# Optimization experiments

Measured on AMD Instinct MI355X. Metric: run time of the kernel, lower is better.

## Reference

```python
import jax, jax.numpy as jnp
import numpy as np

N = 50000
NEG_SLOPE = 0.2

def _gat_layer(x, src, dst, W, a_src, a_dst, b):
    # x: [N, Fin], W: [Fin, Fout], a_src/a_dst: [Fout], b: [Fout]
    h = x @ W                                  # [N, Fout]
    alpha_src = h @ a_src                      # [N]
    alpha_dst = h @ a_dst                      # [N]
    e = alpha_src[src] + alpha_dst[dst]        # [E]
    e = jnp.where(e > 0, e, NEG_SLOPE * e)     # leaky_relu
    # segment softmax over incoming edges of each dst node
    m = jax.ops.segment_max(e, dst, num_segments=N)
    w = jnp.exp(e - m[dst])
    denom = jax.ops.segment_sum(w, dst, num_segments=N) + jnp.asarray(1e-16, e.dtype)
    alpha = w / denom[dst]                     # [E]
    out = jax.ops.segment_sum(alpha[:, None] * h[src], dst, num_segments=N)
    return out + b

def setup_inputs() -> dict:
    key = jax.random.key(0)
    ks = jax.random.split(key, 10)
    x = jax.random.normal(ks[0], (N, 128), dtype=jnp.float32)
    edge_index = jax.random.randint(ks[1], (2, 800000), 0, N, dtype=jnp.int64)
    def glorot(k, shape):
        fan = shape[0] + (shape[1] if len(shape) > 1 else 1)
        s = jnp.sqrt(6.0 / fan)
        return jax.random.uniform(k, shape, jnp.float32, -s, s)
    return {
        "x": x,
        "edge_index": edge_index,
        "W1": glorot(ks[2], (128, 64)),
        "a1_src": glorot(ks[3], (64,)),
        "a1_dst": glorot(ks[4], (64,)),
        "b1": jnp.zeros((64,), jnp.float32),
        "W2": glorot(ks[5], (64, 64)),
        "a2_src": glorot(ks[6], (64,)),
        "a2_dst": glorot(ks[7], (64,)),
        "b2": jnp.zeros((64,), jnp.float32),
    }

def reference(x, edge_index, W1, a1_src, a1_dst, b1, W2, a2_src, a2_dst, b2):
    loops = jnp.arange(N, dtype=edge_index.dtype)
    src = jnp.concatenate([edge_index[0], loops])  # add self-loops (PyG default)
    dst = jnp.concatenate([edge_index[1], loops])
    h = _gat_layer(x, src, dst, W1, a1_src, a1_dst, b1)
    h = jax.nn.relu(h)
    out = _gat_layer(h, src, dst, W2, a2_src, a2_dst, b2)
    return out
```

## Files before the change

### kernel.cpp

```cpp
#include <hip/hip_runtime.h>
#include <hip/hip_bf16.h>
#include <hip/hip_fp16.h>
#include <cstddef>


#define NNODES 50000
#define NEDGES 800000
#define FOUT   64
#define NBKT   512
#define BSPAN  98
#define CHUNK  4096
#define REGS   2560
#define NLBMAX 256

__device__ __forceinline__ float leaky(float t) { return t > 0.f ? t : 0.2f * t; }
#define RL(v, j) __builtin_amdgcn_readlane((v), (j))

using half8  = __attribute__((ext_vector_type(8))) _Float16;
using half4v = __attribute__((ext_vector_type(4))) _Float16;
using f32x4  = __attribute__((ext_vector_type(4))) float;


__global__ __launch_bounds__(256) void k_localsort(
    const int* __restrict__ ei, unsigned* __restrict__ gout,
    int* __restrict__ goff, int E)
{
    __shared__ unsigned lrec[CHUNK];
    __shared__ unsigned lsrt[CHUNK];
    __shared__ int cnt[NBKT];
    __shared__ int cur[NBKT];
    __shared__ int exc[NBKT + 1];

    const int t = threadIdx.x;
    const int blk = blockIdx.x;
    const int e0 = blk * CHUNK;
    const int e1 = min(e0 + CHUNK, E);
    const int ne = e1 - e0;

    for (int i = t; i < NBKT; i += 256) cnt[i] = 0;
    __syncthreads();

    for (int i = e0 + t; i < e1; i += 256) {
        unsigned s = (unsigned)ei[i];
        unsigned d = (unsigned)ei[E + i];
        lrec[i - e0] = s | (d << 16);
        atomicAdd(&cnt[d / BSPAN], 1);
    }
    __syncthreads();

    if (t < 64) {
        int c[8]; int s = 0;
        #pragma unroll
        for (int k = 0; k < 8; ++k) { c[k] = cnt[t * 8 + k]; s += c[k]; }
        int inc = s;
        #pragma unroll
        for (int d = 1; d < 64; d <<= 1) { int u = __shfl_up(inc, d); if (t >= d) inc += u; }
        int ex = inc - s;
        #pragma unroll
        for (int k = 0; k < 8; ++k) { exc[t * 8 + k] = ex; cur[t * 8 + k] = ex; ex += c[k]; }
        if (t == 63) exc[NBKT] = ex;
    }
    __syncthreads();

    for (int i = t; i < ne; i += 256) {
        unsigned r = lrec[i];
        unsigned d = r >> 16;
        unsigned b = d / BSPAN;
        int p = atomicAdd(&cur[b], 1);
        lsrt[p] = (r & 0xFFFFu) | ((d - b * BSPAN) << 16);
    }
    __syncthreads();

    for (int i = t; i < ne; i += 256) gout[e0 + i] = lsrt[i];
    for (int i = t; i < NBKT + 1; i += 256)
        goff[blk * (NBKT + 1) + i] = e0 + exc[i];
}


__device__ __forceinline__ void csr_body(
    char* smem, int bkt,
    const unsigned* __restrict__ gout, const int* __restrict__ goff,
    int* __restrict__ csrc, int2* __restrict__ rowse,
    int n, int nlb)
{
    unsigned* ltmp  = (unsigned*)smem;
    int* lout  = (int*)(smem + REGS * 4);
    int* lcnt  = (int*)(smem + 2 * REGS * 4);
    int* lbase = lcnt + BSPAN;
    int* lcur  = lbase + BSPAN + 1;
    int* rg0   = lcur + BSPAN;
    int* rlen  = rg0 + NLBMAX;
    int* rbase = rlen + NLBMAX;

    const int t = threadIdx.x;
    const int node0 = bkt * BSPAN;
    if (node0 >= n) return;
    const int nn = min(BSPAN, n - node0);

    for (int i = t; i < BSPAN; i += 256) lcnt[i] = (i < nn) ? 1 : 0;
    if (t < nlb) {
        int g0 = goff[t * (NBKT + 1) + bkt];
        int g1 = goff[t * (NBKT + 1) + bkt + 1];
        rg0[t] = g0;
        rlen[t] = g1 - g0;
    }
    __syncthreads();

    if (t < 64) {
        int c[4]; int s = 0;
        #pragma unroll
        for (int k = 0; k < 4; ++k) {
            int idx = t * 4 + k;
            c[k] = (idx < nlb) ? rlen[idx] : 0;
            s += c[k];
        }
        int inc = s;
        #pragma unroll
        for (int d = 1; d < 64; d <<= 1) { int u = __shfl_up(inc, d); if (t >= d) inc += u; }
        int ex = inc - s;
        #pragma unroll
        for (int k = 0; k < 4; ++k) { rbase[t * 4 + k] = ex; ex += c[k]; }
        if (t == 63) rbase[NLBMAX] = ex;
    }
    __syncthreads();

    const int tot = min(rbase[nlb], REGS - BSPAN);

    for (int i = t; i < tot; i += 256) {
        int lo = 0, hi = nlb;
        while (hi - lo > 1) {
            int mid = (lo + hi) >> 1;
            if (rbase[mid] <= i) lo = mid; else hi = mid;
        }
        ltmp[i] = gout[rg0[lo] + (i - rbase[lo])];
    }
    __syncthreads();

    for (int i = t; i < tot; i += 256) atomicAdd(&lcnt[ltmp[i] >> 16], 1);
    __syncthreads();

    if (t < 64) {
        int b0 = t * 2, b1 = t * 2 + 1;
        int c0 = (b0 < BSPAN) ? lcnt[b0] : 0;
        int c1 = (b1 < BSPAN) ? lcnt[b1] : 0;
        int s = c0 + c1;
        int inc = s;
        #pragma unroll
        for (int d = 1; d < 64; d <<= 1) { int u = __shfl_up(inc, d); if (t >= d) inc += u; }
        int ex = inc - s;
        if (b0 < BSPAN) { lbase[b0] = ex;      lcur[b0] = ex + 1; }
        if (b1 < BSPAN) { lbase[b1] = ex + c0; lcur[b1] = ex + c0 + 1; }
        if (t == 63) lbase[BSPAN] = inc;
    }
    __syncthreads();

    for (int i = t; i < nn; i += 256) lout[lbase[i]] = node0 + i;
    for (int i = t; i < tot; i += 256) {
        unsigned r = ltmp[i];
        int p = atomicAdd(&lcur[r >> 16], 1);
        lout[p] = (int)(r & 0xFFFFu);
    }
    __syncthreads();

    const int gbase = bkt * REGS;
    const int total = tot + nn;
    for (int i = t; i < total; i += 256) csrc[gbase + i] = lout[i];
    for (int i = t; i < nn; i += 256)
        rowse[node0 + i] = make_int2(gbase + lbase[i], gbase + lbase[i + 1]);
}


template <int K, typename XT>
__device__ __forceinline__ void gemm_body(
    char* smem, int bx,
    const XT* __restrict__ x, const float* __restrict__ W,
    const float* __restrict__ a_src, const float* __restrict__ a_dst,
    __half* __restrict__ h16, float* __restrict__ as_, float* __restrict__ ad_, int n)
{
    constexpr int KP = K + 8;
    _Float16* Ah = (_Float16*)smem;
    _Float16* Wf = (_Float16*)(smem + 64 * KP * 2);

    const int t    = threadIdx.x;
    const int lane = t & 63;
    const int wv   = t >> 6;
    const int n16  = lane & 15;
    const int quad = lane >> 4;
    const int r0   = bx * 64;

    for (int i = t; i < K * 64; i += 256) {
        int k = i >> 6, c = i & 63;
        Wf[((k >> 3) * 64 + c) * 8 + (k & 7)] = (_Float16)W[i];
    }
    if constexpr (sizeof(XT) == 4) {
        constexpr int KQ = K / 4;
        for (int i = t; i < 64 * KQ; i += 256) {
            int r = i / KQ, kq = i % KQ;
            int row = r0 + r;
            float4 v = make_float4(0.f, 0.f, 0.f, 0.f);
            if (row < n) v = ((const float4*)(x + (size_t)row * K))[kq];
            half4v hv = { (_Float16)v.x, (_Float16)v.y, (_Float16)v.z, (_Float16)v.w };
            *(half4v*)&Ah[r * KP + kq * 4] = hv;
        }
    } else {
        constexpr int KO = K / 8;
        for (int i = t; i < 64 * KO; i += 256) {
            int r = i / KO, ko = i % KO;
            int row = r0 + r;
            half8 hv = {};
            if (row < n) hv = *(const half8*)((const _Float16*)x + (size_t)row * K + ko * 8);
            *(half8*)&Ah[r * KP + ko * 8] = hv;
        }
    }
    __syncthreads();

    half8 bfr[K / 32][4];
    #pragma unroll
    for (int kk = 0; kk < K / 32; ++kk)
        #pragma unroll
        for (int ct = 0; ct < 4; ++ct)
            bfr[kk][ct] = *(const half8*)&Wf[((kk * 4 + quad) * 64 + ct * 16 + n16) * 8];

    f32x4 acc[4];
    #pragma unroll
    for (int ct = 0; ct < 4; ++ct) acc[ct] = (f32x4){0.f, 0.f, 0.f, 0.f};

    #pragma unroll
    for (int kk = 0; kk < K / 32; ++kk) {
        half8 a = *(const half8*)&Ah[(wv * 16 + n16) * KP + kk * 32 + quad * 8];
        #pragma unroll
        for (int ct = 0; ct < 4; ++ct)
            acc[ct] = __builtin_amdgcn_mfma_f32_16x16x32_f16(a, bfr[kk][ct], acc[ct], 0, 0, 0);
    }

    const int rowb = r0 + wv * 16 + quad * 4;
    float asv[4], adv[4];
    #pragma unroll
    for (int ct = 0; ct < 4; ++ct) {
        asv[ct] = a_src[ct * 16 + n16];
        adv[ct] = a_dst[ct * 16 + n16];
    }
    float pa[4] = {0.f, 0.f, 0.f, 0.f}, pd[4] = {0.f, 0.f, 0.f, 0.f};
    #pragma unroll
    for (int ct = 0; ct < 4; ++ct)
        #pragma unroll
        for (int r = 0; r < 4; ++r) {
            pa[r] = fmaf(acc[ct][r], asv[ct], pa[r]);
            pd[r] = fmaf(acc[ct][r], adv[ct], pd[r]);
        }
    #pragma unroll
    for (int r = 0; r < 4; ++r) {
        #pragma unroll
        for (int d = 1; d <= 8; d <<= 1) {
            pa[r] += __shfl_xor(pa[r], d);
            pd[r] += __shfl_xor(pd[r], d);
        }
    }
    if (n16 == 0) {
        #pragma unroll
        for (int r = 0; r < 4; ++r) {
            if (rowb + r < n) { as_[rowb + r] = pa[r]; ad_[rowb + r] = pd[r]; }
        }
    }

    _Float16* hh = (_Float16*)h16;
    #pragma unroll
    for (int r = 0; r < 4; ++r) {
        if (rowb + r < n) {
            #pragma unroll
            for (int ct = 0; ct < 4; ++ct)
                hh[(size_t)(rowb + r) * 64 + ct * 16 + n16] = (_Float16)acc[ct][r];
        }
    }
}


__global__ __launch_bounds__(256) void k_csr_gemm1(
    const unsigned* __restrict__ gout, const int* __restrict__ goff,
    int* __restrict__ csrc, int2* __restrict__ rowse, int nlb,
    const float* __restrict__ x, const float* __restrict__ W1,
    const float* __restrict__ a1s, const float* __restrict__ a1d,
    __half* __restrict__ h16, float* __restrict__ as_, float* __restrict__ ad_, int n)
{
    extern __shared__ __align__(16) char smem[];
    if (blockIdx.x < NBKT)
        csr_body(smem, blockIdx.x, gout, goff, csrc, rowse, n, nlb);
    else
        gemm_body<128, float>(smem, blockIdx.x - NBKT, x, W1, a1s, a1d, h16, as_, ad_, n);
}


__device__ __forceinline__ void agg_one_lds(
    int rloc, int start, int end, float adn, int lane, int2* __restrict__ swrow,
    const int* __restrict__ csrc, const __half* __restrict__ h16,
    const float* __restrict__ as_, const float* __restrict__ bias,
    _Float16* __restrict__ Ah)
{
    constexpr int KP = 72;
    const int deg = end - start;

    if (deg <= 64) {
        int s = 0;
        if (lane < deg) s = csrc[start + lane];
        swrow[lane].x = s << 6;

        const int g  = lane >> 3;
        const int fl = (lane & 7) << 3;
        const __half* __restrict__ hf = h16 + fl;
        const int niter = (deg + 7) >> 3;

        uint4 v[8];
        #pragma unroll
        for (int j = 0; j < 8; ++j)
            if (j < niter) v[j] = *(const uint4*)(hf + swrow[(j << 3) + g].x);

        float e = -1e30f;
        if (lane < deg) e = leaky(as_[s] + adn);
        float w = __expf(e);
        float dsum = w;
        #pragma unroll
        for (int d = 32; d >= 1; d >>= 1) dsum += __shfl_xor(dsum, d);
        swrow[lane].y = __float_as_int(w);

        float af[8] = {0.f, 0.f, 0.f, 0.f, 0.f, 0.f, 0.f, 0.f};
        #pragma unroll
        for (int j = 0; j < 8; ++j) {
            if (j < niter) {
                float wj = __int_as_float(swrow[(j << 3) + g].y);
                unsigned uu[4] = {v[j].x, v[j].y, v[j].z, v[j].w};
                #pragma unroll
                for (int q = 0; q < 4; ++q) {
                    __half2 h2 = *(__half2*)&uu[q];
                    float2 f2 = __half22float2(h2);
                    af[2 * q]     = fmaf(wj, f2.x, af[2 * q]);
                    af[2 * q + 1] = fmaf(wj, f2.y, af[2 * q + 1]);
                }
            }
        }
        #pragma unroll
        for (int q = 0; q < 8; ++q) {
            af[q] += __shfl_xor(af[q], 8);
            af[q] += __shfl_xor(af[q], 16);
            af[q] += __shfl_xor(af[q], 32);
        }
        if (g == 0) {
            float inv = 1.f / dsum;
            float4 b0 = *(const float4*)(bias + fl);
            float4 b1 = *(const float4*)(bias + fl + 4);
            float o[8] = { fmaf(af[0], inv, b0.x), fmaf(af[1], inv, b0.y),
                           fmaf(af[2], inv, b0.z), fmaf(af[3], inv, b0.w),
                           fmaf(af[4], inv, b1.x), fmaf(af[5], inv, b1.y),
                           fmaf(af[6], inv, b1.z), fmaf(af[7], inv, b1.w) };
            half8 st = { (_Float16)fmaxf(o[0], 0.f), (_Float16)fmaxf(o[1], 0.f),
                         (_Float16)fmaxf(o[2], 0.f), (_Float16)fmaxf(o[3], 0.f),
                         (_Float16)fmaxf(o[4], 0.f), (_Float16)fmaxf(o[5], 0.f),
                         (_Float16)fmaxf(o[6], 0.f), (_Float16)fmaxf(o[7], 0.f) };
            *(half8*)&Ah[rloc * KP + fl] = st;
        }
    } else {
        const __half* __restrict__ hp = h16 + lane;
        float m = -1e30f;
        for (int base = start; base < end; base += 64) {
            int idx = base + lane;
            if (idx < end) m = fmaxf(m, leaky(as_[csrc[idx]] + adn));
        }
        #pragma unroll
        for (int d = 32; d >= 1; d >>= 1) m = fmaxf(m, __shfl_xor(m, d));

        float acc0 = 0.f, acc1 = 0.f, acc2 = 0.f, acc3 = 0.f, dsum = 0.f;
        for (int base = start; base < end; base += 64) {
            int idx = base + lane;
            int s = 0; float w = 0.f;
            if (idx < end) {
                s = csrc[idx];
                w = __expf(leaky(as_[s] + adn) - m);
            }
            dsum += w;
            int off = s << 6;
            int wu = __float_as_uint(w);
            int cnt = min(64, end - base);
            int cr = (cnt + 3) & ~3;
            for (int j = 0; j < cr; j += 4) {
                int   o0 = RL(off, j + 0), o1 = RL(off, j + 1);
                int   o2 = RL(off, j + 2), o3 = RL(off, j + 3);
                float w0 = __uint_as_float(RL(wu, j + 0));
                float w1 = __uint_as_float(RL(wu, j + 1));
                float w2 = __uint_as_float(RL(wu, j + 2));
                float w3 = __uint_as_float(RL(wu, j + 3));
                float v0 = __half2float(hp[o0]), v1 = __half2float(hp[o1]);
                float v2 = __half2float(hp[o2]), v3 = __half2float(hp[o3]);
                acc0 = fmaf(w0, v0, acc0);
                acc1 = fmaf(w1, v1, acc1);
                acc2 = fmaf(w2, v2, acc2);
                acc3 = fmaf(w3, v3, acc3);
            }
        }
        #pragma unroll
        for (int d = 32; d >= 1; d >>= 1) dsum += __shfl_xor(dsum, d);
        float acc = (acc0 + acc1) + (acc2 + acc3);
        float o = acc / dsum + bias[lane];
        Ah[rloc * KP + lane] = (_Float16)fmaxf(o, 0.f);
    }
}


__global__ __launch_bounds__(256) void k_agg1_gemm2(
    const int2* __restrict__ rowse, const int* __restrict__ csrc,
    const __half* __restrict__ h1, const float* __restrict__ as1,
    const float* __restrict__ ad1, const float* __restrict__ bias1,
    const float* __restrict__ W2, const float* __restrict__ a2s,
    const float* __restrict__ a2d, __half* __restrict__ h2,
    float* __restrict__ as2, float* __restrict__ ad2, int n)
{
    constexpr int KP = 72;
    __shared__ _Float16 Ah[64 * KP];
    __shared__ _Float16 Wf[64 * 64];
    __shared__ int2 swL[4][64];

    const int t    = threadIdx.x;
    const int lane = t & 63;
    const int wv   = t >> 6;
    const int r0   = blockIdx.x * 64;

    for (int i = t; i < 64 * 64; i += 256) {
        int k = i >> 6, c = i & 63;
        Wf[((k >> 3) * 64 + c) * 8 + (k & 7)] = (_Float16)W2[i];
    }
    if (r0 + 64 > n) {
        for (int i = t; i < 64 * KP; i += 256) Ah[i] = (_Float16)0.f;
    }
    __syncthreads();

    const int half = lane >> 5;
    const int hl   = lane & 31;

    int2  myse = make_int2(0, 0);
    float myad = 0.f;
    {
        int nd = r0 + wv * 16 + lane;
        if (lane < 16 && nd < n) { myse = rowse[nd]; myad = ad1[nd]; }
    }

    for (int it = 0; it < 8; ++it) {
        const int pbase = r0 + wv * 16 + it * 2;
        if (pbase >= n) break;
        const int idx   = it * 2 + half;
        const int start = __shfl(myse.x, idx);
        const int end   = __shfl(myse.y, idx);
        const float adn = __shfl(myad, idx);
        const int deg   = end - start;
        const int rloc  = wv * 16 + it * 2 + half;
        const int mdeg  = max(deg, __shfl_xor(deg, 32));

        if (mdeg <= 32) {
            int s = 0;
            const bool act = hl < deg;
            if (act) s = csrc[start + hl];
            swL[wv][lane].x = s << 6;

            const int g  = (lane >> 3) & 3;
            const int fl = (lane & 7) << 3;
            const __half* __restrict__ hf = h1 + fl;
            int nit = (deg + 3) >> 2;
            nit = max(nit, __shfl_xor(nit, 32));

            const int sbase = (half << 5) + g;
            uint4 v[8];
            #pragma unroll
            for (int j = 0; j < 8; ++j)
                if (j < nit) v[j] = *(const uint4*)(hf + swL[wv][sbase + (j << 2)].x);

            float e = -1e30f;
            if (act) e = leaky(as1[s] + adn);
            float w = __expf(e);
            float dsum = w;
            #pragma unroll
            for (int d = 16; d >= 1; d >>= 1) dsum += __shfl_xor(dsum, d);
            swL[wv][lane].y = __float_as_int(w);

            float af[8] = {0.f, 0.f, 0.f, 0.f, 0.f, 0.f, 0.f, 0.f};
            #pragma unroll
            for (int j = 0; j < 8; ++j) {
                if (j < nit) {
                    float wj = __int_as_float(swL[wv][sbase + (j << 2)].y);
                    unsigned uu[4] = {v[j].x, v[j].y, v[j].z, v[j].w};
                    #pragma unroll
                    for (int q = 0; q < 4; ++q) {
                        __half2 hh2 = *(__half2*)&uu[q];
                        float2 f2 = __half22float2(hh2);
                        af[2 * q]     = fmaf(wj, f2.x, af[2 * q]);
                        af[2 * q + 1] = fmaf(wj, f2.y, af[2 * q + 1]);
                    }
                }
            }
            #pragma unroll
            for (int q = 0; q < 8; ++q) {
                af[q] += __shfl_xor(af[q], 8);
                af[q] += __shfl_xor(af[q], 16);
            }
            if (g == 0) {
                float inv = 1.f / dsum;
                float4 b0 = *(const float4*)(bias1 + fl);
                float4 b1 = *(const float4*)(bias1 + fl + 4);
                float o[8] = { fmaf(af[0], inv, b0.x), fmaf(af[1], inv, b0.y),
                               fmaf(af[2], inv, b0.z), fmaf(af[3], inv, b0.w),
                               fmaf(af[4], inv, b1.x), fmaf(af[5], inv, b1.y),
                               fmaf(af[6], inv, b1.z), fmaf(af[7], inv, b1.w) };
                half8 st = { (_Float16)fmaxf(o[0], 0.f), (_Float16)fmaxf(o[1], 0.f),
                             (_Float16)fmaxf(o[2], 0.f), (_Float16)fmaxf(o[3], 0.f),
                             (_Float16)fmaxf(o[4], 0.f), (_Float16)fmaxf(o[5], 0.f),
                             (_Float16)fmaxf(o[6], 0.f), (_Float16)fmaxf(o[7], 0.f) };
                *(half8*)&Ah[rloc * KP + fl] = st;
            }
        } else {
            int   sA = __shfl(myse.x, it * 2),     eA = __shfl(myse.y, it * 2);
            int   sB = __shfl(myse.x, it * 2 + 1), eB = __shfl(myse.y, it * 2 + 1);
            float aA = __shfl(myad, it * 2),       aB = __shfl(myad, it * 2 + 1);
            agg_one_lds(wv * 16 + it * 2,     sA, eA, aA, lane, swL[wv], csrc, h1, as1, bias1, Ah);
            agg_one_lds(wv * 16 + it * 2 + 1, sB, eB, aB, lane, swL[wv], csrc, h1, as1, bias1, Ah);
        }
    }
    __syncthreads();

    const int n16  = lane & 15;
    const int quad = lane >> 4;

    half8 bfr[2][4];
    #pragma unroll
    for (int kk = 0; kk < 2; ++kk)
        #pragma unroll
        for (int ct = 0; ct < 4; ++ct)
            bfr[kk][ct] = *(const half8*)&Wf[((kk * 4 + quad) * 64 + ct * 16 + n16) * 8];

    f32x4 acc[4];
    #pragma unroll
    for (int ct = 0; ct < 4; ++ct) acc[ct] = (f32x4){0.f, 0.f, 0.f, 0.f};

    #pragma unroll
    for (int kk = 0; kk < 2; ++kk) {
        half8 a = *(const half8*)&Ah[(wv * 16 + n16) * KP + kk * 32 + quad * 8];
        #pragma unroll
        for (int ct = 0; ct < 4; ++ct)
            acc[ct] = __builtin_amdgcn_mfma_f32_16x16x32_f16(a, bfr[kk][ct], acc[ct], 0, 0, 0);
    }

    const int rowb = r0 + wv * 16 + quad * 4;
    float asv[4], adv[4];
    #pragma unroll
    for (int ct = 0; ct < 4; ++ct) {
        asv[ct] = a2s[ct * 16 + n16];
        adv[ct] = a2d[ct * 16 + n16];
    }
    float pa[4] = {0.f, 0.f, 0.f, 0.f}, pd[4] = {0.f, 0.f, 0.f, 0.f};
    #pragma unroll
    for (int ct = 0; ct < 4; ++ct)
        #pragma unroll
        for (int r = 0; r < 4; ++r) {
            pa[r] = fmaf(acc[ct][r], asv[ct], pa[r]);
            pd[r] = fmaf(acc[ct][r], adv[ct], pd[r]);
        }
    #pragma unroll
    for (int r = 0; r < 4; ++r) {
        #pragma unroll
        for (int d = 1; d <= 8; d <<= 1) {
            pa[r] += __shfl_xor(pa[r], d);
            pd[r] += __shfl_xor(pd[r], d);
        }
    }
    if (n16 == 0) {
        #pragma unroll
        for (int r = 0; r < 4; ++r) {
            if (rowb + r < n) { as2[rowb + r] = pa[r]; ad2[rowb + r] = pd[r]; }
        }
    }

    _Float16* hh = (_Float16*)h2;
    #pragma unroll
    for (int r = 0; r < 4; ++r) {
        if (rowb + r < n) {
            #pragma unroll
            for (int ct = 0; ct < 4; ++ct)
                hh[(size_t)(rowb + r) * 64 + ct * 16 + n16] = (_Float16)acc[ct][r];
        }
    }
}


template <bool RELU, typename OT>
__device__ __forceinline__ void agg_one(
    int node, int lane, int2* __restrict__ swrow,
    const int2* __restrict__ rowse,
    const int* __restrict__ csrc, const __half* __restrict__ h16,
    const float* __restrict__ as_, const float* __restrict__ ad_,
    const float* __restrict__ bias, OT* __restrict__ out)
{
    const int2 se = rowse[node];
    const int start = se.x;
    const int end   = se.y;
    const int deg   = end - start;
    const float adn = ad_[node];

    if (deg <= 64) {
        int s = 0;
        if (lane < deg) s = csrc[start + lane];
        swrow[lane].x = s << 6;

        const int g  = lane >> 3;
        const int fl = (lane & 7) << 3;
        const __half* __restrict__ hf = h16 + fl;
        const int niter = (deg + 7) >> 3;

        int sofs[8];
        uint4 v[8];
        #pragma unroll
        for (int j = 0; j < 8; ++j) {
            if (j < niter) {
                sofs[j] = swrow[(j << 3) + g].x;
                v[j] = *(const uint4*)(hf + sofs[j]);
            }
        }

        float e = -1e30f;
        if (lane < deg) e = leaky(as_[s] + adn);
        float w = __expf(e);
        float dsum = w;
        #pragma unroll
        for (int d = 32; d >= 1; d >>= 1) dsum += __shfl_xor(dsum, d);
        swrow[lane].y = __float_as_int(w);

        float af[8] = {0.f, 0.f, 0.f, 0.f, 0.f, 0.f, 0.f, 0.f};
        #pragma unroll
        for (int j = 0; j < 8; ++j) {
            if (j < niter) {
                float wj = __int_as_float(swrow[(j << 3) + g].y);
                unsigned uu[4] = {v[j].x, v[j].y, v[j].z, v[j].w};
                #pragma unroll
                for (int q = 0; q < 4; ++q) {
                    __half2 h2 = *(__half2*)&uu[q];
                    float2 f2 = __half22float2(h2);
                    af[2 * q]     = fmaf(wj, f2.x, af[2 * q]);
                    af[2 * q + 1] = fmaf(wj, f2.y, af[2 * q + 1]);
                }
            }
        }
        #pragma unroll
        for (int q = 0; q < 8; ++q) {
            af[q] += __shfl_xor(af[q], 8);
            af[q] += __shfl_xor(af[q], 16);
            af[q] += __shfl_xor(af[q], 32);
        }
        if (g == 0) {
            float inv = 1.f / dsum;
            float4 b0 = *(const float4*)(bias + fl);
            float4 b1 = *(const float4*)(bias + fl + 4);
            float o[8] = { fmaf(af[0], inv, b0.x), fmaf(af[1], inv, b0.y),
                           fmaf(af[2], inv, b0.z), fmaf(af[3], inv, b0.w),
                           fmaf(af[4], inv, b1.x), fmaf(af[5], inv, b1.y),
                           fmaf(af[6], inv, b1.z), fmaf(af[7], inv, b1.w) };
            if (RELU) {
                #pragma unroll
                for (int q = 0; q < 8; ++q) o[q] = fmaxf(o[q], 0.f);
            }
            if constexpr (sizeof(OT) == 2) {
                __half* op = (__half*)out + (size_t)node * 64 + fl;
                __half2 p0 = __floats2half2_rn(o[0], o[1]);
                __half2 p1 = __floats2half2_rn(o[2], o[3]);
                __half2 p2 = __floats2half2_rn(o[4], o[5]);
                __half2 p3 = __floats2half2_rn(o[6], o[7]);
                uint4 pk = { *(unsigned*)&p0, *(unsigned*)&p1, *(unsigned*)&p2, *(unsigned*)&p3 };
                *(uint4*)op = pk;
            } else {
                float* op = (float*)out + (size_t)node * 64 + fl;
                *(float4*)op       = make_float4(o[0], o[1], o[2], o[3]);
                *(float4*)(op + 4) = make_float4(o[4], o[5], o[6], o[7]);
            }
        }
    } else {
        const __half* __restrict__ hp = h16 + lane;
        float m = -1e30f;
        for (int base = start; base < end; base += 64) {
            int idx = base + lane;
            if (idx < end) m = fmaxf(m, leaky(as_[csrc[idx]] + adn));
        }
        #pragma unroll
        for (int d = 32; d >= 1; d >>= 1) m = fmaxf(m, __shfl_xor(m, d));

        float acc0 = 0.f, acc1 = 0.f, acc2 = 0.f, acc3 = 0.f, dsum = 0.f;
        for (int base = start; base < end; base += 64) {
            int idx = base + lane;
            int s = 0; float w = 0.f;
            if (idx < end) {
                s = csrc[idx];
                w = __expf(leaky(as_[s] + adn) - m);
            }
            dsum += w;
            int off = s << 6;
            int wu = __float_as_uint(w);
            int cnt = min(64, end - base);
            int cr = (cnt + 3) & ~3;
            for (int j = 0; j < cr; j += 4) {
                int   o0 = RL(off, j + 0), o1 = RL(off, j + 1);
                int   o2 = RL(off, j + 2), o3 = RL(off, j + 3);
                float w0 = __uint_as_float(RL(wu, j + 0));
                float w1 = __uint_as_float(RL(wu, j + 1));
                float w2 = __uint_as_float(RL(wu, j + 2));
                float w3 = __uint_as_float(RL(wu, j + 3));
                float v0 = __half2float(hp[o0]), v1 = __half2float(hp[o1]);
                float v2 = __half2float(hp[o2]), v3 = __half2float(hp[o3]);
                acc0 = fmaf(w0, v0, acc0);
                acc1 = fmaf(w1, v1, acc1);
                acc2 = fmaf(w2, v2, acc2);
                acc3 = fmaf(w3, v3, acc3);
            }
        }
        #pragma unroll
        for (int d = 32; d >= 1; d >>= 1) dsum += __shfl_xor(dsum, d);
        float acc = (acc0 + acc1) + (acc2 + acc3);
        float o = acc / dsum + bias[lane];
        if (RELU) o = fmaxf(o, 0.f);
        if constexpr (sizeof(OT) == 2)
            ((__half*)out)[(size_t)node * 64 + lane] = __float2half(o);
        else
            ((float*)out)[(size_t)node * 64 + lane] = o;
    }
}

template <bool RELU, typename OT>
__global__ __launch_bounds__(256) void k_aggregate(
    const int2* __restrict__ rowse,
    const int* __restrict__ csrc,
    const __half* __restrict__ h16, const float* __restrict__ as_,
    const float* __restrict__ ad_, const float* __restrict__ bias,
    OT* __restrict__ out, int n)
{
    __shared__ int2 swL[4][64];

    const int lane = threadIdx.x & 63;
    const int wid  = threadIdx.x >> 6;
    const int nodeA = (blockIdx.x * 4 + wid) * 2;
    if (nodeA >= n) return;

    const int half = lane >> 5;
    const int hl   = lane & 31;
    const int node = nodeA + half;

    const int2 se = rowse[node];
    const float adn = ad_[node];
    const int start = se.x;
    const int deg   = se.y - se.x;
    const int mdeg  = max(deg, __shfl_xor(deg, 32));

    if (mdeg <= 32) {
        int s = 0;
        const bool act = hl < deg;
        if (act) s = csrc[start + hl];
        swL[wid][lane].x = s << 6;

        const int g  = (lane >> 3) & 3;
        const int fl = (lane & 7) << 3;
        const __half* __restrict__ hf = h16 + fl;
        int nit = (deg + 3) >> 2;
        nit = max(nit, __shfl_xor(nit, 32));

        const int sbase = (half << 5) + g;
        uint4 v[8];
        #pragma unroll
        for (int j = 0; j < 8; ++j) {
            if (j < nit)
                v[j] = *(const uint4*)(hf + swL[wid][sbase + (j << 2)].x);
        }

        float e = -1e30f;
        if (act) e = leaky(as_[s] + adn);
        float w = __expf(e);
        float dsum = w;
        #pragma unroll
        for (int d = 16; d >= 1; d >>= 1) dsum += __shfl_xor(dsum, d);
        swL[wid][lane].y = __float_as_int(w);

        float af[8] = {0.f, 0.f, 0.f, 0.f, 0.f, 0.f, 0.f, 0.f};
        #pragma unroll
        for (int j = 0; j < 8; ++j) {
            if (j < nit) {
                float wj = __int_as_float(swL[wid][sbase + (j << 2)].y);
                unsigned uu[4] = {v[j].x, v[j].y, v[j].z, v[j].w};
                #pragma unroll
                for (int q = 0; q < 4; ++q) {
                    __half2 h2 = *(__half2*)&uu[q];
                    float2 f2 = __half22float2(h2);
                    af[2 * q]     = fmaf(wj, f2.x, af[2 * q]);
                    af[2 * q + 1] = fmaf(wj, f2.y, af[2 * q + 1]);
                }
            }
        }
        #pragma unroll
        for (int q = 0; q < 8; ++q) {
            af[q] += __shfl_xor(af[q], 8);
            af[q] += __shfl_xor(af[q], 16);
        }
        if (g == 0) {
            float inv = 1.f / dsum;
            float4 b0 = *(const float4*)(bias + fl);
            float4 b1 = *(const float4*)(bias + fl + 4);
            float o[8] = { fmaf(af[0], inv, b0.x), fmaf(af[1], inv, b0.y),
                           fmaf(af[2], inv, b0.z), fmaf(af[3], inv, b0.w),
                           fmaf(af[4], inv, b1.x), fmaf(af[5], inv, b1.y),
                           fmaf(af[6], inv, b1.z), fmaf(af[7], inv, b1.w) };
            if (RELU) {
                #pragma unroll
                for (int q = 0; q < 8; ++q) o[q] = fmaxf(o[q], 0.f);
            }
            if constexpr (sizeof(OT) == 2) {
                __half* op = (__half*)out + (size_t)node * 64 + fl;
                __half2 p0 = __floats2half2_rn(o[0], o[1]);
                __half2 p1 = __floats2half2_rn(o[2], o[3]);
                __half2 p2 = __floats2half2_rn(o[4], o[5]);
                __half2 p3 = __floats2half2_rn(o[6], o[7]);
                uint4 pk = { *(unsigned*)&p0, *(unsigned*)&p1, *(unsigned*)&p2, *(unsigned*)&p3 };
                *(uint4*)op = pk;
            } else {
                float* op = (float*)out + (size_t)node * 64 + fl;
                *(float4*)op       = make_float4(o[0], o[1], o[2], o[3]);
                *(float4*)(op + 4) = make_float4(o[4], o[5], o[6], o[7]);
            }
        }
    } else {
        agg_one<RELU, OT>(nodeA,     lane, swL[wid], rowse, csrc, h16, as_, ad_, bias, out);
        agg_one<RELU, OT>(nodeA + 1, lane, swL[wid], rowse, csrc, h16, as_, ad_, bias, out);
    }
}


extern "C" void kernel_launch(void* const* d_in, const int* in_sizes, int n_in,
                              void* d_out, int out_size, void* d_ws, size_t ws_size,
                              hipStream_t stream) {
    const float* x   = (const float*)d_in[0];
    const int*   ei  = (const int*)  d_in[1];
    const float* W1  = (const float*)d_in[2];
    const float* a1s = (const float*)d_in[3];
    const float* a1d = (const float*)d_in[4];
    const float* b1  = (const float*)d_in[5];
    const float* W2  = (const float*)d_in[6];
    const float* a2s = (const float*)d_in[7];
    const float* a2d = (const float*)d_in[8];
    const float* b2  = (const float*)d_in[9];
    float* out = (float*)d_out;

    const int N_ = NNODES, E_ = NEDGES;
    const int NLB = (E_ + CHUNK - 1) / CHUNK;

    char* ws = (char*)d_ws;
    size_t off = 0;
    auto alloc = [&](size_t bytes) -> void* {
        void* p = ws + off;
        off += (bytes + 255) & ~(size_t)255;
        return p;
    };
    int*      csrc     = (int*)alloc((size_t)NBKT * REGS * 4);
    int2*     rowse    = (int2*)alloc((size_t)N_ * 8);
    float*    as_      = (float*)alloc((size_t)N_ * 4);
    float*    ad_      = (float*)alloc((size_t)N_ * 4);
    float*    as2      = (float*)alloc((size_t)N_ * 4);
    float*    ad2      = (float*)alloc((size_t)N_ * 4);
    __half*   h16      = (__half*)alloc((size_t)N_ * FOUT * 2);
    __half*   h2       = (__half*)alloc((size_t)N_ * FOUT * 2);
    unsigned* gout     = (unsigned*)alloc((size_t)E_ * 4);
    int*      goff     = (int*)alloc((size_t)NLB * (NBKT + 1) * 4);

    constexpr unsigned SM_G1 = 64 * (128 + 8) * 2 + 128 * 64 * 2;

    const int GB = (N_ + 63) / 64;
    const int AB = (N_ / 2 + 3) / 4;

    k_localsort<<<NLB, 256, 0, stream>>>(ei, gout, goff, E_);
    k_csr_gemm1<<<NBKT + GB, 256, SM_G1, stream>>>(gout, goff, csrc, rowse, NLB,
                                                   x, W1, a1s, a1d, h16, as_, ad_, N_);
    k_agg1_gemm2<<<GB, 256, 0, stream>>>(rowse, csrc, h16, as_, ad_, b1,
                                         W2, a2s, a2d, h2, as2, ad2, N_);
    k_aggregate<false, float><<<AB, 256, 0, stream>>>(rowse, csrc, h2, as2, ad2, b2, out, N_);
}
```

Before: 167.9 us.

## Replace block-tiled MFMA second GEMM with per-wave fp32 matvec fused into aggregation

The layer-1 aggregation kernel no longer collects 64 rows in LDS and runs an MFMA GEMM with W2. Each wave now aggregates two nodes and immediately multiplies each result by W2, held in LDS as fp32, using readlane broadcasts. It then writes h2 and the attention projections directly. This removes the block-wide barrier, the fp16 staging tile and the MFMA phase, and allows smaller blocks (AB grid) with finer load balance. In exchange it does 64 scalar FMAs per output with readlane per node instead of tensor-core work, and uses fp32 rather than fp16 for the matmul.

```diff
diff --git a/kernel.cpp b/kernel.cpp
--- a/kernel.cpp
+++ b/kernel.cpp
@@ -15,6 +15,7 @@
 
 __device__ __forceinline__ float leaky(float t) { return t > 0.f ? t : 0.2f * t; }
 #define RL(v, j) __builtin_amdgcn_readlane((v), (j))
+#define RLF(v, j) __int_as_float(__builtin_amdgcn_readlane(__float_as_int(v), (j)))
 
 using half8  = __attribute__((ext_vector_type(8))) _Float16;
 using half4v = __attribute__((ext_vector_type(4))) _Float16;
@@ -290,14 +291,24 @@
 }
 
 
-__device__ __forceinline__ void agg_one_lds(
-    int rloc, int start, int end, float adn, int lane, int2* __restrict__ swrow,
+__device__ __forceinline__ void agg_one_mv(
+    int node, int lane, int2* __restrict__ swrow,
+    const int2* __restrict__ rowse,
     const int* __restrict__ csrc, const __half* __restrict__ h16,
-    const float* __restrict__ as_, const float* __restrict__ bias,
-    _Float16* __restrict__ Ah)
+    const float* __restrict__ as_, const float* __restrict__ ad_,
+    const float* __restrict__ bias,
+    const float* __restrict__ W2s,
+    const float* __restrict__ a2s, const float* __restrict__ a2d,
+    __half* __restrict__ h2, float* __restrict__ as2, float* __restrict__ ad2)
 {
-    constexpr int KP = 72;
-    const int deg = end - start;
+    const int2 se = rowse[node];
+    const int start = se.x;
+    const int end   = se.y;
+    const int deg   = end - start;
+    const float adn = ad_[node];
+    const float* wcol = W2s + lane;
+
+    float acc2 = 0.f;
 
     if (deg <= 64) {
         int s = 0;
@@ -313,6 +324,257 @@
         #pragma unroll
         for (int j = 0; j < 8; ++j)
             if (j < niter) v[j] = *(const uint4*)(hf + swrow[(j << 3) + g].x);
+
+        float e = -1e30f;
+        if (lane < deg) e = leaky(as_[s] + adn);
+        float w = __expf(e);
+        float dsum = w;
+        #pragma unroll
+        for (int d = 32; d >= 1; d >>= 1) dsum += __shfl_xor(dsum, d);
+        swrow[lane].y = __float_as_int(w);
+
+        float af[8] = {0.f, 0.f, 0.f, 0.f, 0.f, 0.f, 0.f, 0.f};
+        #pragma unroll
+        for (int j = 0; j < 8; ++j) {
+            if (j < niter) {
+                float wj = __int_as_float(swrow[(j << 3) + g].y);
+                unsigned uu[4] = {v[j].x, v[j].y, v[j].z, v[j].w};
+                #pragma unroll
+                for (int q = 0; q < 4; ++q) {
+                    __half2 h2v = *(__half2*)&uu[q];
+                    float2 f2 = __half22float2(h2v);
+                    af[2 * q]     = fmaf(wj, f2.x, af[2 * q]);
+                    af[2 * q + 1] = fmaf(wj, f2.y, af[2 * q + 1]);
+                }
+            }
+        }
+        #pragma unroll
+        for (int q = 0; q < 8; ++q) {
+            af[q] += __shfl_xor(af[q], 8);
+            af[q] += __shfl_xor(af[q], 16);
+            af[q] += __shfl_xor(af[q], 32);
+        }
+        float inv = 1.f / dsum;
+        float4 b0 = *(const float4*)(bias + fl);
+        float4 b1 = *(const float4*)(bias + fl + 4);
+        float o[8] = { fmaxf(fmaf(af[0], inv, b0.x), 0.f), fmaxf(fmaf(af[1], inv, b0.y), 0.f),
+                       fmaxf(fmaf(af[2], inv, b0.z), 0.f), fmaxf(fmaf(af[3], inv, b0.w), 0.f),
+                       fmaxf(fmaf(af[4], inv, b1.x), 0.f), fmaxf(fmaf(af[5], inv, b1.y), 0.f),
+                       fmaxf(fmaf(af[6], inv, b1.z), 0.f), fmaxf(fmaf(af[7], inv, b1.w), 0.f) };
+        #pragma unroll
+        for (int k = 0; k < 64; ++k)
+            acc2 = fmaf(RLF(o[k & 7], k >> 3), wcol[k * 64], acc2);
+    } else {
+        const __half* __restrict__ hp = h16 + lane;
+        float m = -1e30f;
+        for (int base = start; base < end; base += 64) {
+            int idx = base + lane;
+            if (idx < end) m = fmaxf(m, leaky(as_[csrc[idx]] + adn));
+        }
+        #pragma unroll
+        for (int d = 32; d >= 1; d >>= 1) m = fmaxf(m, __shfl_xor(m, d));
+
+        float acc0 = 0.f, acc1 = 0.f, accA = 0.f, accB = 0.f, dsum = 0.f;
+        for (int base = start; base < end; base += 64) {
+            int idx = base + lane;
+            int s = 0; float w = 0.f;
+            if (idx < end) {
+                s = csrc[idx];
+                w = __expf(leaky(as_[s] + adn) - m);
+            }
+            dsum += w;
+            int off = s << 6;
+            int wu = __float_as_uint(w);
+            int cnt = min(64, end - base);
+            int cr = (cnt + 3) & ~3;
+            for (int j = 0; j < cr; j += 4) {
+                int   o0 = RL(off, j + 0), o1 = RL(off, j + 1);
+                int   o2 = RL(off, j + 2), o3 = RL(off, j + 3);
+                float w0 = __uint_as_float(RL(wu, j + 0));
+                float w1 = __uint_as_float(RL(wu, j + 1));
+                float w2 = __uint_as_float(RL(wu, j + 2));
+                float w3 = __uint_as_float(RL(wu, j + 3));
+                float v0 = __half2float(hp[o0]), v1 = __half2float(hp[o1]);
+                float v2 = __half2float(hp[o2]), v3 = __half2float(hp[o3]);
+                acc0 = fmaf(w0, v0, acc0);
+                acc1 = fmaf(w1, v1, acc1);
+                accA = fmaf(w2, v2, accA);
+                accB = fmaf(w3, v3, accB);
+            }
+        }
+        #pragma unroll
+        for (int d = 32; d >= 1; d >>= 1) dsum += __shfl_xor(dsum, d);
+        float acc = (acc0 + acc1) + (accA + accB);
+        float o = fmaxf(acc / dsum + bias[lane], 0.f);
+        #pragma unroll
+        for (int k = 0; k < 64; ++k)
+            acc2 = fmaf(RLF(o, k), wcol[k * 64], acc2);
+    }
+
+    h2[(size_t)node * 64 + lane] = __float2half(acc2);
+    float pa = acc2 * a2s[lane];
+    float pd = acc2 * a2d[lane];
+    #pragma unroll
+    for (int d = 32; d >= 1; d >>= 1) {
+        pa += __shfl_xor(pa, d);
+        pd += __shfl_xor(pd, d);
+    }
+    if (lane == 0) { as2[node] = pa; ad2[node] = pd; }
+}
+
+__global__ __launch_bounds__(256) void k_agg1mv(
+    const int2* __restrict__ rowse,
+    const int* __restrict__ csrc,
+    const __half* __restrict__ h16, const float* __restrict__ as_,
+    const float* __restrict__ ad_, const float* __restrict__ bias,
+    const float* __restrict__ W2, const float* __restrict__ a2s,
+    const float* __restrict__ a2d,
+    __half* __restrict__ h2, float* __restrict__ as2, float* __restrict__ ad2, int n)
+{
+    __shared__ float W2s[64 * 64];
+    __shared__ int2 swL[4][64];
+
+    const int t = threadIdx.x;
+    for (int i = t; i < 64 * 64; i += 256) W2s[i] = W2[i];
+    __syncthreads();
+
+    const int lane = t & 63;
+    const int wid  = t >> 6;
+    const int nodeA = (blockIdx.x * 4 + wid) * 2;
+    if (nodeA >= n) return;
+
+    const int half = lane >> 5;
+    const int hl   = lane & 31;
+    const int node = nodeA + half;
+
+    const int2 se = rowse[node];
+    const float adn = ad_[node];
+    const int start = se.x;
+    const int deg   = se.y - se.x;
+    const int mdeg  = max(deg, __shfl_xor(deg, 32));
+
+    if (mdeg <= 32) {
+        int s = 0;
+        const bool act = hl < deg;
+        if (act) s = csrc[start + hl];
+        swL[wid][lane].x = s << 6;
+
+        const int g  = (lane >> 3) & 3;
+        const int fl = (lane & 7) << 3;
+        const __half* __restrict__ hf = h16 + fl;
+        int nit = (deg + 3) >> 2;
+        nit = max(nit, __shfl_xor(nit, 32));
+
+        const int sbase = (half << 5) + g;
+        uint4 v[8];
+        #pragma unroll
+        for (int j = 0; j < 8; ++j) {
+            if (j < nit)
+                v[j] = *(const uint4*)(hf + swL[wid][sbase + (j << 2)].x);
+        }
+
+        float e = -1e30f;
+        if (act) e = leaky(as_[s] + adn);
+        float w = __expf(e);
+        float dsum = w;
+        #pragma unroll
+        for (int d = 16; d >= 1; d >>= 1) dsum += __shfl_xor(dsum, d);
+        swL[wid][lane].y = __float_as_int(w);
+
+        float af[8] = {0.f, 0.f, 0.f, 0.f, 0.f, 0.f, 0.f, 0.f};
+        #pragma unroll
+        for (int j = 0; j < 8; ++j) {
+            if (j < nit) {
+                float wj = __int_as_float(swL[wid][sbase + (j << 2)].y);
+                unsigned uu[4] = {v[j].x, v[j].y, v[j].z, v[j].w};
+                #pragma unroll
+                for (int q = 0; q < 4; ++q) {
+                    __half2 h2v = *(__half2*)&uu[q];
+                    float2 f2 = __half22float2(h2v);
+                    af[2 * q]     = fmaf(wj, f2.x, af[2 * q]);
+                    af[2 * q + 1] = fmaf(wj, f2.y, af[2 * q + 1]);
+                }
+            }
+        }
+        #pragma unroll
+        for (int q = 0; q < 8; ++q) {
+            af[q] += __shfl_xor(af[q], 8);
+            af[q] += __shfl_xor(af[q], 16);
+        }
+        float inv = 1.f / dsum;
+        float4 b0 = *(const float4*)(bias + fl);
+        float4 b1 = *(const float4*)(bias + fl + 4);
+        float o[8] = { fmaxf(fmaf(af[0], inv, b0.x), 0.f), fmaxf(fmaf(af[1], inv, b0.y), 0.f),
+                       fmaxf(fmaf(af[2], inv, b0.z), 0.f), fmaxf(fmaf(af[3], inv, b0.w), 0.f),
+                       fmaxf(fmaf(af[4], inv, b1.x), 0.f), fmaxf(fmaf(af[5], inv, b1.y), 0.f),
+                       fmaxf(fmaf(af[6], inv, b1.z), 0.f), fmaxf(fmaf(af[7], inv, b1.w), 0.f) };
+
+        const float* wcol = W2s + lane;
+        const float s2 = a2s[lane];
+        const float d2 = a2d[lane];
+        float accA = 0.f, accB = 0.f;
+        #pragma unroll
+        for (int k = 0; k < 64; ++k) {
+            float wv = wcol[k * 64];
+            accA = fmaf(RLF(o[k & 7], k >> 3), wv, accA);
+            accB = fmaf(RLF(o[k & 7], 32 + (k >> 3)), wv, accB);
+        }
+        h2[(size_t)nodeA * 64 + lane]       = __float2half(accA);
+        h2[(size_t)(nodeA + 1) * 64 + lane] = __float2half(accB);
+
+        float pa = accA * s2, pd = accA * d2;
+        float qa = accB * s2, qd = accB * d2;
+        #pragma unroll
+        for (int d = 32; d >= 1; d >>= 1) {
+            pa += __shfl_xor(pa, d);
+            pd += __shfl_xor(pd, d);
+            qa += __shfl_xor(qa, d);
+            qd += __shfl_xor(qd, d);
+        }
+        if (lane == 0) {
+            as2[nodeA] = pa;     ad2[nodeA] = pd;
+            as2[nodeA + 1] = qa; ad2[nodeA + 1] = qd;
+        }
+    } else {
+        agg_one_mv(nodeA,     lane, swL[wid], rowse, csrc, h16, as_, ad_, bias,
+                   W2s, a2s, a2d, h2, as2, ad2);
+        agg_one_mv(nodeA + 1, lane, swL[wid], rowse, csrc, h16, as_, ad_, bias,
+                   W2s, a2s, a2d, h2, as2, ad2);
+    }
+}
+
+
+template <bool RELU, typename OT>
+__device__ __forceinline__ void agg_one(
+    int node, int lane, int2* __restrict__ swrow,
+    const int2* __restrict__ rowse,
+    const int* __restrict__ csrc, const __half* __restrict__ h16,
+    const float* __restrict__ as_, const float* __restrict__ ad_,
+    const float* __restrict__ bias, OT* __restrict__ out)
+{
+    const int2 se = rowse[node];
+    const int start = se.x;
+    const int end   = se.y;
+    const int deg   = end - start;
+    const float adn = ad_[node];
+
+    if (deg <= 64) {
+        int s = 0;
+        if (lane < deg) s = csrc[start + lane];
+        swrow[lane].x = s << 6;
+
+        const int g  = lane >> 3;
+        const int fl = (lane & 7) << 3;
+        const __half* __restrict__ hf = h16 + fl;
+        const int niter = (deg + 7) >> 3;
+
+        uint4 v[8];
+        #pragma unroll
+        for (int j = 0; j < 8; ++j) {
+            if (j < niter) {
+                v[j] = *(const uint4*)(hf + swrow[(j << 3) + g].x);
+            }
+        }
 
         float e = -1e30f;
         if (lane < deg) e = leaky(as_[s] + adn);
@@ -351,11 +613,23 @@
                            fmaf(af[2], inv, b0.z), fmaf(af[3], inv, b0.w),
                            fmaf(af[4], inv, b1.x), fmaf(af[5], inv, b1.y),
                            fmaf(af[6], inv, b1.z), fmaf(af[7], inv, b1.w) };
-            half8 st = { (_Float16)fmaxf(o[0], 0.f), (_Float16)fmaxf(o[1], 0.f),
-                         (_Float16)fmaxf(o[2], 0.f), (_Float16)fmaxf(o[3], 0.f),
-                         (_Float16)fmaxf(o[4], 0.f), (_Float16)fmaxf(o[5], 0.f),
-                         (_Float16)fmaxf(o[6], 0.f), (_Float16)fmaxf(o[7], 0.f) };
-            *(half8*)&Ah[rloc * KP + fl] = st;
+            if (RELU) {
+                #pragma unroll
+                for (int q = 0; q < 8; ++q) o[q] = fmaxf(o[q], 0.f);
+            }
+            if constexpr (sizeof(OT) == 2) {
+                __half* op = (__half*)out + (size_t)node * 64 + fl;
+                __half2 p0 = __floats2half2_rn(o[0], o[1]);
+                __half2 p1 = __floats2half2_rn(o[2], o[3]);
+                __half2 p2 = __floats2half2_rn(o[4], o[5]);
+                __half2 p3 = __floats2half2_rn(o[6], o[7]);
+                uint4 pk = { *(unsigned*)&p0, *(unsigned*)&p1, *(unsigned*)&p2, *(unsigned*)&p3 };
+                *(uint4*)op = pk;
+            } else {
+                float* op = (float*)out + (size_t)node * 64 + fl;
+                *(float4*)op       = make_float4(o[0], o[1], o[2], o[3]);
+                *(float4*)(op + 4) = make_float4(o[4], o[5], o[6], o[7]);
+            }
         }
     } else {
         const __half* __restrict__ hp = h16 + lane;
@@ -399,324 +673,6 @@
         for (int d = 32; d >= 1; d >>= 1) dsum += __shfl_xor(dsum, d);
         float acc = (acc0 + acc1) + (acc2 + acc3);
         float o = acc / dsum + bias[lane];
-        Ah[rloc * KP + lane] = (_Float16)fmaxf(o, 0.f);
-    }
-}
-
-
-__global__ __launch_bounds__(256) void k_agg1_gemm2(
-    const int2* __restrict__ rowse, const int* __restrict__ csrc,
-    const __half* __restrict__ h1, const float* __restrict__ as1,
-    const float* __restrict__ ad1, const float* __restrict__ bias1,
-    const float* __restrict__ W2, const float* __restrict__ a2s,
-    const float* __restrict__ a2d, __half* __restrict__ h2,
-    float* __restrict__ as2, float* __restrict__ ad2, int n)
-{
-    constexpr int KP = 72;
-    __shared__ _Float16 Ah[64 * KP];
-    __shared__ _Float16 Wf[64 * 64];
-    __shared__ int2 swL[4][64];
-
-    const int t    = threadIdx.x;
-    const int lane = t & 63;
-    const int wv   = t >> 6;
-    const int r0   = blockIdx.x * 64;
-
-    for (int i = t; i < 64 * 64; i += 256) {
-        int k = i >> 6, c = i & 63;
-        Wf[((k >> 3) * 64 + c) * 8 + (k & 7)] = (_Float16)W2[i];
-    }
-    if (r0 + 64 > n) {
-        for (int i = t; i < 64 * KP; i += 256) Ah[i] = (_Float16)0.f;
-    }
-    __syncthreads();
-
-    const int half = lane >> 5;
-    const int hl   = lane & 31;
-
-    int2  myse = make_int2(0, 0);
-    float myad = 0.f;
-    {
-        int nd = r0 + wv * 16 + lane;
-        if (lane < 16 && nd < n) { myse = rowse[nd]; myad = ad1[nd]; }
-    }
-
-    for (int it = 0; it < 8; ++it) {
-        const int pbase = r0 + wv * 16 + it * 2;
-        if (pbase >= n) break;
-        const int idx   = it * 2 + half;
-        const int start = __shfl(myse.x, idx);
-        const int end   = __shfl(myse.y, idx);
-        const float adn = __shfl(myad, idx);
-        const int deg   = end - start;
-        const int rloc  = wv * 16 + it * 2 + half;
-        const int mdeg  = max(deg, __shfl_xor(deg, 32));
-
-        if (mdeg <= 32) {
-            int s = 0;
-            const bool act = hl < deg;
-            if (act) s = csrc[start + hl];
-            swL[wv][lane].x = s << 6;
-
-            const int g  = (lane >> 3) & 3;
-            const int fl = (lane & 7) << 3;
-            const __half* __restrict__ hf = h1 + fl;
-            int nit = (deg + 3) >> 2;
-            nit = max(nit, __shfl_xor(nit, 32));
-
-            const int sbase = (half << 5) + g;
-            uint4 v[8];
-            #pragma unroll
-            for (int j = 0; j < 8; ++j)
-                if (j < nit) v[j] = *(const uint4*)(hf + swL[wv][sbase + (j << 2)].x);
-
-            float e = -1e30f;
-            if (act) e = leaky(as1[s] + adn);
-            float w = __expf(e);
-            float dsum = w;
-            #pragma unroll
-            for (int d = 16; d >= 1; d >>= 1) dsum += __shfl_xor(dsum, d);
-            swL[wv][lane].y = __float_as_int(w);
-
-            float af[8] = {0.f, 0.f, 0.f, 0.f, 0.f, 0.f, 0.f, 0.f};
-            #pragma unroll
-            for (int j = 0; j < 8; ++j) {
-                if (j < nit) {
-                    float wj = __int_as_float(swL[wv][sbase + (j << 2)].y);
-                    unsigned uu[4] = {v[j].x, v[j].y, v[j].z, v[j].w};
-                    #pragma unroll
-                    for (int q = 0; q < 4; ++q) {
-                        __half2 hh2 = *(__half2*)&uu[q];
-                        float2 f2 = __half22float2(hh2);
-                        af[2 * q]     = fmaf(wj, f2.x, af[2 * q]);
-                        af[2 * q + 1] = fmaf(wj, f2.y, af[2 * q + 1]);
-                    }
-                }
-            }
-            #pragma unroll
-            for (int q = 0; q < 8; ++q) {
-                af[q] += __shfl_xor(af[q], 8);
-                af[q] += __shfl_xor(af[q], 16);
-            }
-            if (g == 0) {
-                float inv = 1.f / dsum;
-                float4 b0 = *(const float4*)(bias1 + fl);
-                float4 b1 = *(const float4*)(bias1 + fl + 4);
-                float o[8] = { fmaf(af[0], inv, b0.x), fmaf(af[1], inv, b0.y),
-                               fmaf(af[2], inv, b0.z), fmaf(af[3], inv, b0.w),
-                               fmaf(af[4], inv, b1.x), fmaf(af[5], inv, b1.y),
-                               fmaf(af[6], inv, b1.z), fmaf(af[7], inv, b1.w) };
-                half8 st = { (_Float16)fmaxf(o[0], 0.f), (_Float16)fmaxf(o[1], 0.f),
-                             (_Float16)fmaxf(o[2], 0.f), (_Float16)fmaxf(o[3], 0.f),
-                             (_Float16)fmaxf(o[4], 0.f), (_Float16)fmaxf(o[5], 0.f),
-                             (_Float16)fmaxf(o[6], 0.f), (_Float16)fmaxf(o[7], 0.f) };
-                *(half8*)&Ah[rloc * KP + fl] = st;
-            }
-        } else {
-            int   sA = __shfl(myse.x, it * 2),     eA = __shfl(myse.y, it * 2);
-            int   sB = __shfl(myse.x, it * 2 + 1), eB = __shfl(myse.y, it * 2 + 1);
-            float aA = __shfl(myad, it * 2),       aB = __shfl(myad, it * 2 + 1);
-            agg_one_lds(wv * 16 + it * 2,     sA, eA, aA, lane, swL[wv], csrc, h1, as1, bias1, Ah);
-            agg_one_lds(wv * 16 + it * 2 + 1, sB, eB, aB, lane, swL[wv], csrc, h1, as1, bias1, Ah);
-        }
-    }
-    __syncthreads();
-
-    const int n16  = lane & 15;
-    const int quad = lane >> 4;
-
-    half8 bfr[2][4];
-    #pragma unroll
-    for (int kk = 0; kk < 2; ++kk)
-        #pragma unroll
-        for (int ct = 0; ct < 4; ++ct)
-            bfr[kk][ct] = *(const half8*)&Wf[((kk * 4 + quad) * 64 + ct * 16 + n16) * 8];
-
-    f32x4 acc[4];
-    #pragma unroll
-    for (int ct = 0; ct < 4; ++ct) acc[ct] = (f32x4){0.f, 0.f, 0.f, 0.f};
-
-    #pragma unroll
-    for (int kk = 0; kk < 2; ++kk) {
-        half8 a = *(const half8*)&Ah[(wv * 16 + n16) * KP + kk * 32 + quad * 8];
-        #pragma unroll
-        for (int ct = 0; ct < 4; ++ct)
-            acc[ct] = __builtin_amdgcn_mfma_f32_16x16x32_f16(a, bfr[kk][ct], acc[ct], 0, 0, 0);
-    }
-
-    const int rowb = r0 + wv * 16 + quad * 4;
-    float asv[4], adv[4];
-    #pragma unroll
-    for (int ct = 0; ct < 4; ++ct) {
-        asv[ct] = a2s[ct * 16 + n16];
-        adv[ct] = a2d[ct * 16 + n16];
-    }
-    float pa[4] = {0.f, 0.f, 0.f, 0.f}, pd[4] = {0.f, 0.f, 0.f, 0.f};
-    #pragma unroll
-    for (int ct = 0; ct < 4; ++ct)
-        #pragma unroll
-        for (int r = 0; r < 4; ++r) {
-            pa[r] = fmaf(acc[ct][r], asv[ct], pa[r]);
-            pd[r] = fmaf(acc[ct][r], adv[ct], pd[r]);
-        }
-    #pragma unroll
-    for (int r = 0; r < 4; ++r) {
-        #pragma unroll
-        for (int d = 1; d <= 8; d <<= 1) {
-            pa[r] += __shfl_xor(pa[r], d);
-            pd[r] += __shfl_xor(pd[r], d);
-        }
-    }
-    if (n16 == 0) {
-        #pragma unroll
-        for (int r = 0; r < 4; ++r) {
-            if (rowb + r < n) { as2[rowb + r] = pa[r]; ad2[rowb + r] = pd[r]; }
-        }
-    }
-
-    _Float16* hh = (_Float16*)h2;
-    #pragma unroll
-    for (int r = 0; r < 4; ++r) {
-        if (rowb + r < n) {
-            #pragma unroll
-            for (int ct = 0; ct < 4; ++ct)
-                hh[(size_t)(rowb + r) * 64 + ct * 16 + n16] = (_Float16)acc[ct][r];
-        }
-    }
-}
-
-
-template <bool RELU, typename OT>
-__device__ __forceinline__ void agg_one(
-    int node, int lane, int2* __restrict__ swrow,
-    const int2* __restrict__ rowse,
-    const int* __restrict__ csrc, const __half* __restrict__ h16,
-    const float* __restrict__ as_, const float* __restrict__ ad_,
-    const float* __restrict__ bias, OT* __restrict__ out)
-{
-    const int2 se = rowse[node];
-    const int start = se.x;
-    const int end   = se.y;
-    const int deg   = end - start;
-    const float adn = ad_[node];
-
-    if (deg <= 64) {
-        int s = 0;
-        if (lane < deg) s = csrc[start + lane];
-        swrow[lane].x = s << 6;
-
-        const int g  = lane >> 3;
-        const int fl = (lane & 7) << 3;
-        const __half* __restrict__ hf = h16 + fl;
-        const int niter = (deg + 7) >> 3;
-
-        int sofs[8];
-        uint4 v[8];
-        #pragma unroll
-        for (int j = 0; j < 8; ++j) {
-            if (j < niter) {
-                sofs[j] = swrow[(j << 3) + g].x;
-                v[j] = *(const uint4*)(hf + sofs[j]);
-            }
-        }
-
-        float e = -1e30f;
-        if (lane < deg) e = leaky(as_[s] + adn);
-        float w = __expf(e);
-        float dsum = w;
-        #pragma unroll
-        for (int d = 32; d >= 1; d >>= 1) dsum += __shfl_xor(dsum, d);
-        swrow[lane].y = __float_as_int(w);
-
-        float af[8] = {0.f, 0.f, 0.f, 0.f, 0.f, 0.f, 0.f, 0.f};
-        #pragma unroll
-        for (int j = 0; j < 8; ++j) {
-            if (j < niter) {
-                float wj = __int_as_float(swrow[(j << 3) + g].y);
-                unsigned uu[4] = {v[j].x, v[j].y, v[j].z, v[j].w};
-                #pragma unroll
-                for (int q = 0; q < 4; ++q) {
-                    __half2 h2 = *(__half2*)&uu[q];
-                    float2 f2 = __half22float2(h2);
-                    af[2 * q]     = fmaf(wj, f2.x, af[2 * q]);
-                    af[2 * q + 1] = fmaf(wj, f2.y, af[2 * q + 1]);
-                }
-            }
-        }
-        #pragma unroll
-        for (int q = 0; q < 8; ++q) {
-            af[q] += __shfl_xor(af[q], 8);
-            af[q] += __shfl_xor(af[q], 16);
-            af[q] += __shfl_xor(af[q], 32);
-        }
-        if (g == 0) {
-            float inv = 1.f / dsum;
-            float4 b0 = *(const float4*)(bias + fl);
-            float4 b1 = *(const float4*)(bias + fl + 4);
-            float o[8] = { fmaf(af[0], inv, b0.x), fmaf(af[1], inv, b0.y),
-                           fmaf(af[2], inv, b0.z), fmaf(af[3], inv, b0.w),
-                           fmaf(af[4], inv, b1.x), fmaf(af[5], inv, b1.y),
-                           fmaf(af[6], inv, b1.z), fmaf(af[7], inv, b1.w) };
-            if (RELU) {
-                #pragma unroll
-                for (int q = 0; q < 8; ++q) o[q] = fmaxf(o[q], 0.f);
-            }
-            if constexpr (sizeof(OT) == 2) {
-                __half* op = (__half*)out + (size_t)node * 64 + fl;
-                __half2 p0 = __floats2half2_rn(o[0], o[1]);
-                __half2 p1 = __floats2half2_rn(o[2], o[3]);
-                __half2 p2 = __floats2half2_rn(o[4], o[5]);
-                __half2 p3 = __floats2half2_rn(o[6], o[7]);
-                uint4 pk = { *(unsigned*)&p0, *(unsigned*)&p1, *(unsigned*)&p2, *(unsigned*)&p3 };
-                *(uint4*)op = pk;
-            } else {
-                float* op = (float*)out + (size_t)node * 64 + fl;
-                *(float4*)op       = make_float4(o[0], o[1], o[2], o[3]);
-                *(float4*)(op + 4) = make_float4(o[4], o[5], o[6], o[7]);
-            }
-        }
-    } else {
-        const __half* __restrict__ hp = h16 + lane;
-        float m = -1e30f;
-        for (int base = start; base < end; base += 64) {
-            int idx = base + lane;
-            if (idx < end) m = fmaxf(m, leaky(as_[csrc[idx]] + adn));
-        }
-        #pragma unroll
-        for (int d = 32; d >= 1; d >>= 1) m = fmaxf(m, __shfl_xor(m, d));
-
-        float acc0 = 0.f, acc1 = 0.f, acc2 = 0.f, acc3 = 0.f, dsum = 0.f;
-        for (int base = start; base < end; base += 64) {
-            int idx = base + lane;
-            int s = 0; float w = 0.f;
-            if (idx < end) {
-                s = csrc[idx];
-                w = __expf(leaky(as_[s] + adn) - m);
-            }
-            dsum += w;
-            int off = s << 6;
-            int wu = __float_as_uint(w);
-            int cnt = min(64, end - base);
-            int cr = (cnt + 3) & ~3;
-            for (int j = 0; j < cr; j += 4) {
-                int   o0 = RL(off, j + 0), o1 = RL(off, j + 1);
-                int   o2 = RL(off, j + 2), o3 = RL(off, j + 3);
-                float w0 = __uint_as_float(RL(wu, j + 0));
-                float w1 = __uint_as_float(RL(wu, j + 1));
-                float w2 = __uint_as_float(RL(wu, j + 2));
-                float w3 = __uint_as_float(RL(wu, j + 3));
-                float v0 = __half2float(hp[o0]), v1 = __half2float(hp[o1]);
-                float v2 = __half2float(hp[o2]), v3 = __half2float(hp[o3]);
-                acc0 = fmaf(w0, v0, acc0);
-                acc1 = fmaf(w1, v1, acc1);
-                acc2 = fmaf(w2, v2, acc2);
-                acc3 = fmaf(w3, v3, acc3);
-            }
-        }
-        #pragma unroll
-        for (int d = 32; d >= 1; d >>= 1) dsum += __shfl_xor(dsum, d);
-        float acc = (acc0 + acc1) + (acc2 + acc3);
-        float o = acc / dsum + bias[lane];
         if (RELU) o = fmaxf(o, 0.f);
         if constexpr (sizeof(OT) == 2)
             ((__half*)out)[(size_t)node * 64 + lane] = __float2half(o);
@@ -875,7 +831,7 @@
     k_localsort<<<NLB, 256, 0, stream>>>(ei, gout, goff, E_);
     k_csr_gemm1<<<NBKT + GB, 256, SM_G1, stream>>>(gout, goff, csrc, rowse, NLB,
                                                    x, W1, a1s, a1d, h16, as_, ad_, N_);
-    k_agg1_gemm2<<<GB, 256, 0, stream>>>(rowse, csrc, h16, as_, ad_, b1,
-                                         W2, a2s, a2d, h2, as2, ad2, N_);
+    k_agg1mv<<<AB, 256, 0, stream>>>(rowse, csrc, h16, as_, ad_, b1,
+                                     W2, a2s, a2d, h2, as2, ad2, N_);
     k_aggregate<false, float><<<AB, 256, 0, stream>>>(rowse, csrc, h2, as2, ad2, b2, out, N_);
 }
```

After: 162.9 us. 3.0% less time.
